# Performance work log

Hardware: AMD Instinct MI355X
Metric: run time of the kernel (lower is better)

## Reference

```python
import jax, jax.numpy as jnp
import numpy as np

VAT = 57      # vat_tokens
ACT = 56      # action_num (KV slice start for cross-attn)
H = 16        # num_heads
NG = 3        # n_groups for num_non_act == 768


def setup_inputs() -> dict:
    key = jax.random.key(0)
    ks = jax.random.split(key, 6)
    B, N, C = 64, 825, 1024
    s = 0.02
    return {
        "x": jax.random.normal(ks[0], (B, N, C), dtype=jnp.float32),
        "W_qkv_non": jax.random.normal(ks[1], (C, 3 * C), dtype=jnp.float32) * s,
        "W_q_act": jax.random.normal(ks[2], (C, C), dtype=jnp.float32) * s,
        "W_kv_act": jax.random.normal(ks[3], (C, 2 * C), dtype=jnp.float32) * s,
        "W_proj_non": jax.random.normal(ks[4], (C, C), dtype=jnp.float32) * s,
        "b_proj_non": jnp.zeros((C,), dtype=jnp.float32),
        "W_proj_act": jax.random.normal(ks[5], (C, C), dtype=jnp.float32) * s,
        "b_proj_act": jnp.zeros((C,), dtype=jnp.float32),
    }


def reference(x, W_qkv_non, W_q_act, W_kv_act, W_proj_non, b_proj_non,
              W_proj_act, b_proj_act):
    B, N, C = x.shape
    d = C // H
    scale = d ** -0.5
    nna = N - VAT              # num non-act tokens (768)
    gs = nna // NG             # group size (256)

    # --- grouped windowed self-attention over non-act tokens ---
    non = x[:, VAT:].reshape(B, NG, gs, C)
    qkv = (non @ W_qkv_non).reshape(B, NG, gs, 3, H, d)
    q, k, v = jnp.moveaxis(qkv, 3, 0)           # each [B, NG, gs, H, d]
    q = q.transpose(0, 1, 3, 2, 4)              # [B, NG, H, gs, d]
    k = k.transpose(0, 1, 3, 2, 4)
    v = v.transpose(0, 1, 3, 2, 4)
    attn = jax.nn.softmax(jnp.einsum('bghqd,bghkd->bghqk', q, k) * scale, axis=-1)
    x_non = jnp.einsum('bghqk,bghkd->bghqd', attn, v)
    x_non = x_non.transpose(0, 1, 3, 2, 4).reshape(B, nna, C)

    # --- cross-attention: act queries attend to KV subset [ACT:] of all tokens ---
    q_act = (x[:, :VAT] @ W_q_act).reshape(B, VAT, H, d).transpose(0, 2, 1, 3)
    kv = (x @ W_kv_act).reshape(B, N, 2, H, d)
    k_act = kv[:, ACT:, 0].transpose(0, 2, 1, 3)   # [B, H, N-ACT, d]
    v_act = kv[:, ACT:, 1].transpose(0, 2, 1, 3)
    attn_a = jax.nn.softmax(jnp.einsum('bhqd,bhkd->bhqk', q_act, k_act) * scale, axis=-1)
    x_act = jnp.einsum('bhqk,bhkd->bhqd', attn_a, v_act)
    x_act = x_act.transpose(0, 2, 1, 3).reshape(B, VAT, C)

    # --- output projections + concat [act, non] ---
    x_non = x_non @ W_proj_non + b_proj_non
    x_act = x_act @ W_proj_act + b_proj_act
    return jnp.concatenate([x_act, x_non], axis=1)
```

## Files before the change

kernel.cpp:

```cpp
#include <hip/hip_runtime.h>
#include <stdint.h>


typedef __attribute__((ext_vector_type(8))) unsigned short u16x8;
typedef __attribute__((ext_vector_type(8))) _Float16 f16x8;
typedef __attribute__((ext_vector_type(4))) float f32x4;

__device__ __forceinline__ unsigned short f2h(float f) {
  _Float16 h = (_Float16)f;
  return __builtin_bit_cast(unsigned short, h);
}

__device__ __forceinline__ float exp2r(float x) {
  return __builtin_amdgcn_exp2f(x);
}

__device__ __forceinline__ void mfma16(f32x4& d, u16x8 a, u16x8 b) {
  d = __builtin_amdgcn_mfma_f32_16x16x32_f16(
      __builtin_bit_cast(f16x8, a), __builtin_bit_cast(f16x8, b), d, 0, 0, 0);
}

__device__ __forceinline__ void async16(void* lds_p, const void* g) {
  __builtin_amdgcn_global_load_lds(
      (const __attribute__((address_space(1))) unsigned int*)g,
      (__attribute__((address_space(3))) unsigned int*)lds_p, 16, 0, 0);
}

__device__ __forceinline__ int swz(int row, int bcol) {
  return (row << 7) + (bcol ^ ((row & 7) << 4));
}

__device__ __forceinline__ int xcd_swz(int bid, int nwg) {
  int q8 = nwg >> 3, r8 = nwg & 7;
  int xcd = bid & 7, idx = bid >> 3;
  return (xcd < r8 ? xcd * (q8 + 1) : r8 * (q8 + 1) + (xcd - r8) * q8) + idx;
}

static constexpr size_t OFF_XB   = 0;
static constexpr size_t OFF_QKV  = 108134400;
static constexpr size_t OFF_KV   = 410124288;
static constexpr size_t OFF_QACT = 611713024;
static constexpr size_t OFF_ANON = 619184128;
static constexpr size_t OFF_AACT = 719847424;
static constexpr size_t OFF_WQKV = 727318528;
static constexpr size_t OFF_WKV  = 733609984;
static constexpr size_t OFF_WQ   = 737804288;
static constexpr size_t OFF_WPN  = 739901440;
static constexpr size_t OFF_WPA  = 741998592;

__global__ __launch_bounds__(256) void k_cast(const float* __restrict__ in,
                                              unsigned short* __restrict__ outp,
                                              int n8) {
  int stride = gridDim.x * 256;
  for (int i = blockIdx.x * 256 + threadIdx.x; i < n8; i += stride) {
    float4 v0 = ((const float4*)in)[i * 2];
    float4 v1 = ((const float4*)in)[i * 2 + 1];
    uint4 w;
    w.x = (unsigned)f2h(v0.x) | ((unsigned)f2h(v0.y) << 16);
    w.y = (unsigned)f2h(v0.z) | ((unsigned)f2h(v0.w) << 16);
    w.z = (unsigned)f2h(v1.x) | ((unsigned)f2h(v1.y) << 16);
    w.w = (unsigned)f2h(v1.z) | ((unsigned)f2h(v1.w) << 16);
    ((uint4*)outp)[i] = w;
  }
}

__global__ __launch_bounds__(256) void k_tc5(
    const float* __restrict__ Wqkv, const float* __restrict__ Wkv,
    const float* __restrict__ Wq,   const float* __restrict__ Wpn,
    const float* __restrict__ Wpa,
    unsigned short* __restrict__ Tqkv, unsigned short* __restrict__ Tkv,
    unsigned short* __restrict__ Tq,   unsigned short* __restrict__ Tpn,
    unsigned short* __restrict__ Tpa) {
  __shared__ float ts[32][33];
  int bx = blockIdx.x;
  const float* W; unsigned short* Wt; int Nc, nb;
  if (bx < 96)       { W = Wqkv; Wt = Tqkv; Nc = 3072; nb = bx; }
  else if (bx < 160) { W = Wkv;  Wt = Tkv;  Nc = 2048; nb = bx - 96; }
  else if (bx < 192) { W = Wq;   Wt = Tq;   Nc = 1024; nb = bx - 160; }
  else if (bx < 224) { W = Wpn;  Wt = Tpn;  Nc = 1024; nb = bx - 192; }
  else               { W = Wpa;  Wt = Tpa;  Nc = 1024; nb = bx - 224; }
  int n0 = nb * 32, k0 = blockIdx.y * 32;
  int tx = threadIdx.x & 31, ty = threadIdx.x >> 5;
#pragma unroll
  for (int i = 0; i < 4; i++) {
    int k = ty + i * 8;
    ts[k][tx] = W[(size_t)(k0 + k) * Nc + n0 + tx];
  }
  __syncthreads();
#pragma unroll
  for (int i = 0; i < 4; i++) {
    int n = ty + i * 8;
    Wt[(size_t)(n0 + n) * 1024 + k0 + tx] = f2h(ts[tx][n]);
  }
}

template <int EPI>
__device__ __forceinline__ void gemm256_body(
    const unsigned short* __restrict__ A, const unsigned short* __restrict__ Bt,
    const float* __restrict__ bias, void* __restrict__ outp,
    int M, int NTN, int arpb, int aoff, int ldo, int orpb, int ooff,
    int wg, char* lds) {
  int tid = threadIdx.x, lane = tid & 63, wid = tid >> 6;
  int fr = lane & 15, fg = lane >> 4;

  int mt = wg / NTN, nt = wg - mt * NTN;
  int r0 = mt << 8, n0 = nt << 8;
  if (r0 > M - 256) r0 = M - 256;

  const unsigned short* pA[2][2];
  const unsigned short* pB[2][2];
#pragma unroll
  for (int j = 0; j < 2; j++) {
    int rc = (wid * 2 + j) * 8 + (lane >> 3);
    int cc = (lane & 7) ^ (rc & 7);
#pragma unroll
    for (int a = 0; a < 2; a++) {
      int row = (rc >> 6) * 128 + a * 64 + (rc & 63);
      int r = r0 + row;
      if (r >= M) r = M - 1;
      size_t gr;
      if (arpb > 0) { int bb = r / arpb; gr = (size_t)bb * 825 + aoff + (r - bb * arpb); }
      else gr = (size_t)r;
      pA[a][j] = A + gr * 1024 + cc * 8;
    }
#pragma unroll
    for (int b = 0; b < 2; b++) {
      int n = ((rc >> 5) & 3) * 64 + b * 32 + (rc & 31);
      pB[b][j] = Bt + (size_t)(n0 + n) * 1024 + cc * 8;
    }
  }

  int wr = wid >> 2, wc = wid & 3;
  int ch0 = fg ^ (fr & 7);
  int aoff0 = (wr * 64 + fr) * 128 + ch0 * 16;
  int boff0 = (wc * 32 + fr) * 128 + ch0 * 16;

  u16x8 afr[8], bf0[4], bf1[4];
  f32x4 acc[8][4] = {};

#define BAR  asm volatile("s_barrier" ::: "memory")
#define VM6  asm volatile("s_waitcnt vmcnt(6)" ::: "memory")
#define VM0  asm volatile("s_waitcnt vmcnt(0)" ::: "memory")

  auto LDA = [&](int d, int a) {
    char* base = lds + d * 65536 + a * 16384;
#pragma unroll
    for (int mm = 0; mm < 4; mm++)
#pragma unroll
      for (int ks = 0; ks < 2; ks++)
        afr[mm * 2 + ks] = *(const u16x8*)(base + mm * 2048 + (aoff0 ^ (ks * 64)));
  };
  auto LDB = [&](int d, int b, u16x8* bf) {
    char* base = lds + d * 65536 + 32768 + b * 16384;
#pragma unroll
    for (int nn = 0; nn < 2; nn++)
#pragma unroll
      for (int ks = 0; ks < 2; ks++)
        bf[nn * 2 + ks] = *(const u16x8*)(base + nn * 2048 + (boff0 ^ (ks * 64)));
  };
  auto STAGE_A = [&](int d, int a, int t) {
#pragma unroll
    for (int j = 0; j < 2; j++)
      async16(lds + d * 65536 + a * 16384 + ((wid * 2 + j) << 10), pA[a][j] + t * 64);
  };
  auto STAGE_B = [&](int d, int b, int t) {
#pragma unroll
    for (int j = 0; j < 2; j++)
      async16(lds + d * 65536 + 32768 + b * 16384 + ((wid * 2 + j) << 10), pB[b][j] + t * 64);
  };
  auto CLUSTER = [&](int a, int b, u16x8* bf) {
    __builtin_amdgcn_s_setprio(1);
#pragma unroll
    for (int mm = 0; mm < 4; mm++)
#pragma unroll
      for (int nn = 0; nn < 2; nn++)
#pragma unroll
        for (int ks = 0; ks < 2; ks++)
          mfma16(acc[a * 4 + mm][b * 2 + nn], afr[mm * 2 + ks], bf[nn * 2 + ks]);
    __builtin_amdgcn_s_setprio(0);
  };

  STAGE_A(0, 0, 0); STAGE_B(0, 0, 0); STAGE_B(0, 1, 0); STAGE_A(0, 1, 0);
  STAGE_A(1, 0, 1); STAGE_B(1, 0, 1); STAGE_B(1, 1, 1);
  VM6; BAR;

#pragma unroll 1
  for (int i = 0; i < 8; i++) {
    bool nl = (i < 7);
    int t1 = 2 * i + 1, t2 = 2 * i + 2, t3 = 2 * i + 3;
    LDA(0, 0); LDB(0, 0, bf0);
    STAGE_A(1, 1, t1);
    CLUSTER(0, 0, bf0); BAR;
    LDB(0, 1, bf1);
    if (nl) STAGE_A(0, 0, t2);
    CLUSTER(0, 1, bf1);
    LDA(0, 1);
    if (nl) STAGE_B(0, 0, t2);
    CLUSTER(1, 0, bf0); BAR;
    if (nl) STAGE_B(0, 1, t2);
    CLUSTER(1, 1, bf1);
    if (nl) { VM6; } else { VM0; }
    BAR;
    LDA(1, 0); LDB(1, 0, bf0);
    if (nl) STAGE_A(0, 1, t2);
    CLUSTER(0, 0, bf0); BAR;
    LDB(1, 1, bf1);
    if (nl) STAGE_A(1, 0, t3);
    CLUSTER(0, 1, bf1);
    LDA(1, 1);
    if (nl) STAGE_B(1, 0, t3);
    CLUSTER(1, 0, bf0); BAR;
    if (nl) STAGE_B(1, 1, t3);
    CLUSTER(1, 1, bf1);
    if (nl) { VM6; } else { VM0; }
    BAR;
  }
#undef BAR
#undef VM6
#undef VM0

  int coln[4];
#pragma unroll
  for (int n = 0; n < 4; n++)
    coln[n] = n0 + wc * 64 + (n >> 1) * 32 + (n & 1) * 16 + fr;
  if (EPI == 0) {
    unsigned short* o = (unsigned short*)outp;
#pragma unroll
    for (int m = 0; m < 8; m++)
#pragma unroll
      for (int reg = 0; reg < 4; reg++) {
        int r = r0 + wr * 128 + (m >> 2) * 64 + (m & 3) * 16 + (lane >> 4) * 4 + reg;
        if (r < M) {
          size_t base = (size_t)r * ldo;
#pragma unroll
          for (int n = 0; n < 4; n++) o[base + coln[n]] = f2h(acc[m][n][reg]);
        }
      }
  } else {
    float* o = (float*)outp;
#pragma unroll
    for (int m = 0; m < 8; m++)
#pragma unroll
      for (int reg = 0; reg < 4; reg++) {
        int r = r0 + wr * 128 + (m >> 2) * 64 + (m & 3) * 16 + (lane >> 4) * 4 + reg;
        if (r < M) {
          int bb = r / orpb;
          size_t orow = (size_t)bb * 825 + ooff + (r - bb * orpb);
          size_t base = orow * 1024;
#pragma unroll
          for (int n = 0; n < 4; n++)
            o[base + coln[n]] = acc[m][n][reg] + bias[coln[n]];
        }
      }
  }
}

__global__ __launch_bounds__(512, 2) void k_gemm_in(
    const unsigned short* __restrict__ xb,
    const unsigned short* __restrict__ WtQKV,
    const unsigned short* __restrict__ WtKV,
    const unsigned short* __restrict__ WtQ,
    unsigned short* __restrict__ qkv, unsigned short* __restrict__ kvb,
    unsigned short* __restrict__ qact) {
  extern __shared__ char lds[];
  int bid = blockIdx.x;
  if (bid < 2304) {
    gemm256_body<0>(xb, WtQKV, nullptr, qkv, 49152, 12, 768, 57, 3072, 0, 0,
                    xcd_swz(bid, 2304), lds);
  } else if (bid < 3848) {
    gemm256_body<0>(xb, WtKV, nullptr, kvb, 49216, 8, 769, 56, 2048, 0, 0,
                    xcd_swz(bid - 2304, 1544), lds);
  } else {
    gemm256_body<0>(xb, WtQ, nullptr, qact, 3648, 4, 57, 0, 1024, 0, 0,
                    xcd_swz(bid - 3848, 60), lds);
  }
}

template <int EPI>
__global__ __launch_bounds__(512, 2) void k_gemm256(
    const unsigned short* __restrict__ A, const unsigned short* __restrict__ Bt,
    const float* __restrict__ bias, void* __restrict__ outp,
    int M, int NTN, int arpb, int aoff, int ldo, int orpb, int ooff) {
  extern __shared__ char lds[];
  gemm256_body<EPI>(A, Bt, bias, outp, M, NTN, arpb, aoff, ldo, orpb, ooff,
                    xcd_swz(blockIdx.x, gridDim.x), lds);
}

template <int EPI>
__global__ __launch_bounds__(256, 2) void k_gemm(
    const unsigned short* __restrict__ A, const unsigned short* __restrict__ Bt,
    const float* __restrict__ bias, void* __restrict__ outp,
    int M, int Nn, int arpb, int aoff, int ldo, int orpb, int ooff) {
  __shared__ __align__(16) unsigned short As[128 * 32];
  __shared__ __align__(16) unsigned short Bs[128 * 32];
  int tid = threadIdx.x, lane = tid & 63, wid = tid >> 6;
  int NT = Nn >> 7;
  int mt = blockIdx.x / NT, nt = blockIdx.x - mt * NT;
  int r0 = mt << 7, n0 = nt << 7;

  const unsigned short* aptr[2];
  const unsigned short* bptr[2];
#pragma unroll
  for (int i = 0; i < 2; i++) {
    int c = tid + (i << 8);
    int r = r0 + (c >> 2);
    if (r >= M) r = M - 1;
    size_t gr;
    if (arpb > 0) { int bb = r / arpb; gr = (size_t)bb * 825 + aoff + (r - bb * arpb); }
    else gr = (size_t)r;
    aptr[i] = A + gr * 1024 + (c & 3) * 8;
    bptr[i] = Bt + (size_t)(n0 + (c >> 2)) * 1024 + (c & 3) * 8;
  }
  char* AsB = (char*)As;
  char* BsB = (char*)Bs;
  int wr = wid >> 1, wc = wid & 1;
  int fr = lane & 15, fcol = (lane >> 4) * 16;
  f32x4 acc[4][4] = {};

  for (int kk = 0; kk < 1024; kk += 32) {
    async16(AsB + (wid << 10), aptr[0] + kk);
    async16(AsB + 4096 + (wid << 10), aptr[1] + kk);
    async16(BsB + (wid << 10), bptr[0] + kk);
    async16(BsB + 4096 + (wid << 10), bptr[1] + kk);
    __syncthreads();
    u16x8 af[4], bfv[4];
#pragma unroll
    for (int m = 0; m < 4; m++)
      af[m] = *(const u16x8*)(AsB + (wr * 64 + m * 16 + fr) * 64 + fcol);
#pragma unroll
    for (int n = 0; n < 4; n++)
      bfv[n] = *(const u16x8*)(BsB + (wc * 64 + n * 16 + fr) * 64 + fcol);
#pragma unroll
    for (int m = 0; m < 4; m++)
#pragma unroll
      for (int n = 0; n < 4; n++) mfma16(acc[m][n], af[m], bfv[n]);
    __syncthreads();
  }

  int cb = wc * 64 + fr;
  int rb = wr * 64 + (lane >> 4) * 4;
  if (EPI == 0) {
    unsigned short* o = (unsigned short*)outp;
#pragma unroll
    for (int m = 0; m < 4; m++)
#pragma unroll
      for (int reg = 0; reg < 4; reg++) {
        int r = r0 + rb + m * 16 + reg;
        if (r < M) {
          size_t base = (size_t)r * ldo + n0 + cb;
#pragma unroll
          for (int n = 0; n < 4; n++) o[base + n * 16] = f2h(acc[m][n][reg]);
        }
      }
  } else {
    float* o = (float*)outp;
#pragma unroll
    for (int m = 0; m < 4; m++)
#pragma unroll
      for (int reg = 0; reg < 4; reg++) {
        int r = r0 + rb + m * 16 + reg;
        if (r < M) {
          int bb = r / orpb;
          size_t orow = (size_t)bb * 825 + ooff + (r - bb * orpb);
          size_t base = orow * 1024 + n0 + cb;
#pragma unroll
          for (int n = 0; n < 4; n++)
            o[base + n * 16] = acc[m][n][reg] + bias[n0 + cb + n * 16];
        }
      }
  }
}

__global__ __launch_bounds__(256, 2) void k_attn_non(
    const unsigned short* __restrict__ qkv, unsigned short* __restrict__ aout) {
  int bid = blockIdx.x;
  int h = bid & 15, t = bid >> 4;
  int g = t % 3, b = t / 3;
  int tid = threadIdx.x, lane = tid & 63, wid = tid >> 6;
  int fr = lane & 15, fg = lane >> 4;
  size_t rowbase = (size_t)(b * 768 + g * 256);
  const unsigned short* Qb = qkv + rowbase * 3072 + h * 64;
  const unsigned short* Kb = Qb + 1024;
  const unsigned short* Vb = Qb + 2048;

  __shared__ __align__(16) unsigned short Vts[64 * 64];
  __shared__ __align__(16) unsigned short Ps[4][64 * 64];
  char* VtB = (char*)Vts;
  char* Pw = (char*)Ps[wid];

  int qr = wid * 64;
  u16x8 qf[4][2];
#pragma unroll
  for (int mq = 0; mq < 4; mq++)
#pragma unroll
    for (int ks = 0; ks < 2; ks++)
      qf[mq][ks] = *(const u16x8*)(Qb + (size_t)(qr + mq * 16 + fr) * 3072 + ks * 32 + fg * 8);

  f32x4 o[4][4] = {};
  float mrun[4], lrun[4];
#pragma unroll
  for (int mq = 0; mq < 4; mq++) { mrun[mq] = -1e30f; lrun[mq] = 0.f; }
  const float c1 = 0.125f * 1.44269504089f;

  int vpr = tid >> 3, vcc = tid & 7;
  u16x8 v0 = *(const u16x8*)(Vb + (size_t)(2 * vpr) * 3072 + vcc * 8);
  u16x8 v1 = *(const u16x8*)(Vb + (size_t)(2 * vpr + 1) * 3072 + vcc * 8);
  u16x8 kf[2][4];
#pragma unroll
  for (int kt = 0; kt < 4; kt++)
#pragma unroll
    for (int ks = 0; ks < 2; ks++)
      kf[ks][kt] = *(const u16x8*)(Kb + (size_t)(kt * 16 + fr) * 3072 + ks * 32 + fg * 8);

  for (int c = 0; c < 4; c++) {
    __syncthreads();
#pragma unroll
    for (int j = 0; j < 8; j++) {
      unsigned pk = (unsigned)v0[j] | ((unsigned)v1[j] << 16);
      *(unsigned*)(VtB + swz(vcc * 8 + j, 4 * vpr)) = pk;
    }
    if (c < 3) {
      v0 = *(const u16x8*)(Vb + (size_t)((c + 1) * 64 + 2 * vpr) * 3072 + vcc * 8);
      v1 = *(const u16x8*)(Vb + (size_t)((c + 1) * 64 + 2 * vpr + 1) * 3072 + vcc * 8);
    }

    f32x4 s[4][4] = {};
#pragma unroll
    for (int ks = 0; ks < 2; ks++)
#pragma unroll
      for (int kt = 0; kt < 4; kt++)
#pragma unroll
        for (int mq = 0; mq < 4; mq++) mfma16(s[kt][mq], kf[ks][kt], qf[mq][ks]);
    if (c < 3) {
#pragma unroll
      for (int kt = 0; kt < 4; kt++)
#pragma unroll
        for (int ks = 0; ks < 2; ks++)
          kf[ks][kt] = *(const u16x8*)(Kb + (size_t)((c + 1) * 64 + kt * 16 + fr) * 3072 + ks * 32 + fg * 8);
    }
#pragma unroll
    for (int kt = 0; kt < 4; kt++)
#pragma unroll
      for (int mq = 0; mq < 4; mq++) s[kt][mq] *= c1;

#pragma unroll
    for (int mq = 0; mq < 4; mq++) {
      float v = -1e30f;
#pragma unroll
      for (int kt = 0; kt < 4; kt++)
#pragma unroll
        for (int reg = 0; reg < 4; reg++) v = fmaxf(v, s[kt][mq][reg]);
      v = fmaxf(v, __shfl_xor(v, 16));
      v = fmaxf(v, __shfl_xor(v, 32));
      float mn = fmaxf(mrun[mq], v);
      float alpha = exp2r(mrun[mq] - mn);
      mrun[mq] = mn;
      int q = mq * 16 + fr;
      float rs = 0.f;
#pragma unroll
      for (int kt = 0; kt < 4; kt++) {
        f32x4 p;
#pragma unroll
        for (int reg = 0; reg < 4; reg++) p[reg] = exp2r(s[kt][mq][reg] - mn);
        rs += p[0] + p[1] + p[2] + p[3];
        uint2 w;
        w.x = (unsigned)f2h(p[0]) | ((unsigned)f2h(p[1]) << 16);
        w.y = (unsigned)f2h(p[2]) | ((unsigned)f2h(p[3]) << 16);
        *(uint2*)(Pw + swz(q, kt * 32 + fg * 8)) = w;
      }
      rs += __shfl_xor(rs, 16);
      rs += __shfl_xor(rs, 32);
      lrun[mq] = lrun[mq] * alpha + rs;
#pragma unroll
      for (int dt = 0; dt < 4; dt++) o[dt][mq] *= alpha;
    }
    __syncthreads();
#pragma unroll
    for (int ks = 0; ks < 2; ks++) {
      u16x8 vf[4], pf[4];
#pragma unroll
      for (int dt = 0; dt < 4; dt++)
        vf[dt] = *(const u16x8*)(VtB + swz(dt * 16 + fr, ks * 64 + fg * 16));
#pragma unroll
      for (int mq = 0; mq < 4; mq++)
        pf[mq] = *(const u16x8*)(Pw + swz(mq * 16 + fr, ks * 64 + fg * 16));
#pragma unroll
      for (int dt = 0; dt < 4; dt++)
#pragma unroll
        for (int mq = 0; mq < 4; mq++) mfma16(o[dt][mq], vf[dt], pf[mq]);
    }
  }

#pragma unroll
  for (int mq = 0; mq < 4; mq++) {
    float rl = 1.0f / lrun[mq];
    size_t row = rowbase + qr + mq * 16 + fr;
#pragma unroll
    for (int dt = 0; dt < 4; dt++) {
      uint2 w;
      w.x = (unsigned)f2h(o[dt][mq][0] * rl) | ((unsigned)f2h(o[dt][mq][1] * rl) << 16);
      w.y = (unsigned)f2h(o[dt][mq][2] * rl) | ((unsigned)f2h(o[dt][mq][3] * rl) << 16);
      *(uint2*)(aout + row * 1024 + h * 64 + dt * 16 + fg * 4) = w;
    }
  }
}

__global__ __launch_bounds__(256, 2) void k_attn_act(
    const unsigned short* __restrict__ qa, const unsigned short* __restrict__ kv,
    unsigned short* __restrict__ aout) {
  int bid = blockIdx.x;
  int h = bid & 15, b = bid >> 4;
  int tid = threadIdx.x, lane = tid & 63, wid = tid >> 6;
  int fr = lane & 15, fg = lane >> 4;
  const unsigned short* Qb = qa + (size_t)b * 57 * 1024 + h * 64;
  const unsigned short* Kb = kv + (size_t)b * 769 * 2048 + h * 64;
  const unsigned short* Vb = Kb + 1024;

  __shared__ __align__(16) unsigned short Vts[4][64 * 64];
  __shared__ __align__(16) unsigned short Ps[4][64 * 64];
  __shared__ float Ml[4][64], Ll[4][64];
  char* Vw = (char*)Vts[wid];
  char* Pw = (char*)Ps[wid];

  u16x8 qf[4][2];
#pragma unroll
  for (int mq = 0; mq < 4; mq++) {
    int q = mq * 16 + fr;
    if (q > 56) q = 56;
#pragma unroll
    for (int ks = 0; ks < 2; ks++)
      qf[mq][ks] = *(const u16x8*)(Qb + (size_t)q * 1024 + ks * 32 + fg * 8);
  }
  f32x4 o[4][4] = {};
  float mrun[4], lrun[4];
#pragma unroll
  for (int mq = 0; mq < 4; mq++) { mrun[mq] = -1e30f; lrun[mq] = 0.f; }
  const float c1 = 0.125f * 1.44269504089f;

  u16x8 kf[2][4];
  {
    int kc0 = wid * 64;
#pragma unroll
    for (int kt = 0; kt < 4; kt++) {
      int krow = kc0 + kt * 16 + fr;
      if (krow > 768) krow = 768;
#pragma unroll
      for (int ks = 0; ks < 2; ks++)
        kf[ks][kt] = *(const u16x8*)(Kb + (size_t)krow * 2048 + ks * 32 + fg * 8);
    }
  }

  for (int c = wid; c < 13; c += 4) {
    int kc0 = c * 64;
#pragma unroll
    for (int i = 0; i < 4; i++) {
      int idx = lane + i * 64;
      int pr = idx >> 3, cv = idx & 7;
      int kr0 = kc0 + 2 * pr, kr1 = kc0 + 2 * pr + 1;
      if (kr0 > 768) kr0 = 768;
      if (kr1 > 768) kr1 = 768;
      u16x8 v0 = *(const u16x8*)(Vb + (size_t)kr0 * 2048 + cv * 8);
      u16x8 v1 = *(const u16x8*)(Vb + (size_t)kr1 * 2048 + cv * 8);
#pragma unroll
      for (int j = 0; j < 8; j++) {
        unsigned pk = (unsigned)v0[j] | ((unsigned)v1[j] << 16);
        *(unsigned*)(Vw + swz(cv * 8 + j, 4 * pr)) = pk;
      }
    }

    f32x4 s[4][4] = {};
#pragma unroll
    for (int ks = 0; ks < 2; ks++)
#pragma unroll
      for (int kt = 0; kt < 4; kt++)
#pragma unroll
        for (int mq = 0; mq < 4; mq++) mfma16(s[kt][mq], kf[ks][kt], qf[mq][ks]);
    if (c + 4 < 13) {
      int kn = (c + 4) * 64;
#pragma unroll
      for (int kt = 0; kt < 4; kt++) {
        int krow = kn + kt * 16 + fr;
        if (krow > 768) krow = 768;
#pragma unroll
        for (int ks = 0; ks < 2; ks++)
          kf[ks][kt] = *(const u16x8*)(Kb + (size_t)krow * 2048 + ks * 32 + fg * 8);
      }
    }
#pragma unroll
    for (int kt = 0; kt < 4; kt++)
#pragma unroll
      for (int mq = 0; mq < 4; mq++) s[kt][mq] *= c1;
    if (kc0 + 64 > 769) {
#pragma unroll
      for (int kt = 0; kt < 4; kt++)
#pragma unroll
        for (int reg = 0; reg < 4; reg++)
          if (kc0 + kt * 16 + fg * 4 + reg >= 769)
#pragma unroll
            for (int mq = 0; mq < 4; mq++) s[kt][mq][reg] = -1e30f;
    }

#pragma unroll
    for (int mq = 0; mq < 4; mq++) {
      float v = -1e30f;
#pragma unroll
      for (int kt = 0; kt < 4; kt++)
#pragma unroll
        for (int reg = 0; reg < 4; reg++) v = fmaxf(v, s[kt][mq][reg]);
      v = fmaxf(v, __shfl_xor(v, 16));
      v = fmaxf(v, __shfl_xor(v, 32));
      float mn = fmaxf(mrun[mq], v);
      float alpha = exp2r(mrun[mq] - mn);
      mrun[mq] = mn;
      int q = mq * 16 + fr;
      float rs = 0.f;
#pragma unroll
      for (int kt = 0; kt < 4; kt++) {
        f32x4 p;
#pragma unroll
        for (int reg = 0; reg < 4; reg++) p[reg] = exp2r(s[kt][mq][reg] - mn);
        rs += p[0] + p[1] + p[2] + p[3];
        uint2 w;
        w.x = (unsigned)f2h(p[0]) | ((unsigned)f2h(p[1]) << 16);
        w.y = (unsigned)f2h(p[2]) | ((unsigned)f2h(p[3]) << 16);
        *(uint2*)(Pw + swz(q, kt * 32 + fg * 8)) = w;
      }
      rs += __shfl_xor(rs, 16);
      rs += __shfl_xor(rs, 32);
      lrun[mq] = lrun[mq] * alpha + rs;
#pragma unroll
      for (int dt = 0; dt < 4; dt++) o[dt][mq] *= alpha;
    }
#pragma unroll
    for (int ks = 0; ks < 2; ks++) {
      u16x8 vf[4], pf[4];
#pragma unroll
      for (int dt = 0; dt < 4; dt++)
        vf[dt] = *(const u16x8*)(Vw + swz(dt * 16 + fr, ks * 64 + fg * 16));
#pragma unroll
      for (int mq = 0; mq < 4; mq++)
        pf[mq] = *(const u16x8*)(Pw + swz(mq * 16 + fr, ks * 64 + fg * 16));
#pragma unroll
      for (int dt = 0; dt < 4; dt++)
#pragma unroll
        for (int mq = 0; mq < 4; mq++) mfma16(o[dt][mq], vf[dt], pf[mq]);
    }
  }

  __syncthreads();
  if (fg == 0) {
#pragma unroll
    for (int mq = 0; mq < 4; mq++) {
      Ml[wid][mq * 16 + fr] = mrun[mq];
      Ll[wid][mq * 16 + fr] = lrun[mq];
    }
  }
  __syncthreads();
  float* Oac = (float*)&Vts[0][0];
  for (int i = tid; i < 4096; i += 256) Oac[i] = 0.f;
  __syncthreads();
  for (int w = 0; w < 4; w++) {
    if (wid == w) {
#pragma unroll
      for (int mq = 0; mq < 4; mq++) {
        int q = mq * 16 + fr;
        float Mq = fmaxf(fmaxf(Ml[0][q], Ml[1][q]), fmaxf(Ml[2][q], Ml[3][q]));
        float f = exp2r(mrun[mq] - Mq);
#pragma unroll
        for (int dt = 0; dt < 4; dt++) {
          int d = dt * 16 + fg * 4;
#pragma unroll
          for (int reg = 0; reg < 4; reg++)
            Oac[(d + reg) * 64 + q] += o[dt][mq][reg] * f;
        }
      }
    }
    __syncthreads();
  }
  for (int i = tid; i < 4096; i += 256) {
    int d = i >> 6, q = i & 63;
    if (q < 57) {
      float Mq = fmaxf(fmaxf(Ml[0][q], Ml[1][q]), fmaxf(Ml[2][q], Ml[3][q]));
      float Lq = Ll[0][q] * exp2r(Ml[0][q] - Mq) + Ll[1][q] * exp2r(Ml[1][q] - Mq) +
                 Ll[2][q] * exp2r(Ml[2][q] - Mq) + Ll[3][q] * exp2r(Ml[3][q] - Mq);
      aout[(size_t)(b * 57 + q) * 1024 + h * 64 + d] = f2h(Oac[i] / Lq);
    }
  }
}

extern "C" void kernel_launch(void* const* d_in, const int* in_sizes, int n_in,
                              void* d_out, int out_size, void* d_ws, size_t ws_size,
                              hipStream_t stream) {
  const float* x    = (const float*)d_in[0];
  const float* Wqkv = (const float*)d_in[1];
  const float* Wq   = (const float*)d_in[2];
  const float* Wkv  = (const float*)d_in[3];
  const float* Wpn  = (const float*)d_in[4];
  const float* bpn  = (const float*)d_in[5];
  const float* Wpa  = (const float*)d_in[6];
  const float* bpa  = (const float*)d_in[7];
  float* out = (float*)d_out;
  char* ws = (char*)d_ws;

  unsigned short* xb   = (unsigned short*)(ws + OFF_XB);
  unsigned short* qkv  = (unsigned short*)(ws + OFF_QKV);
  unsigned short* kvb  = (unsigned short*)(ws + OFF_KV);
  unsigned short* qact = (unsigned short*)(ws + OFF_QACT);
  unsigned short* anon = (unsigned short*)(ws + OFF_ANON);
  unsigned short* aact = (unsigned short*)(ws + OFF_AACT);
  unsigned short* WtQKV = (unsigned short*)(ws + OFF_WQKV);
  unsigned short* WtKV  = (unsigned short*)(ws + OFF_WKV);
  unsigned short* WtQ   = (unsigned short*)(ws + OFF_WQ);
  unsigned short* WtPN  = (unsigned short*)(ws + OFF_WPN);
  unsigned short* WtPA  = (unsigned short*)(ws + OFF_WPA);

  hipFuncSetAttribute((const void*)k_gemm_in,
                      hipFuncAttributeMaxDynamicSharedMemorySize, 131072);
  hipFuncSetAttribute((const void*)k_gemm256<1>,
                      hipFuncAttributeMaxDynamicSharedMemorySize, 131072);

  k_cast<<<2048, 256, 0, stream>>>(x, xb, 6758400);
  k_tc5<<<dim3(256, 32), 256, 0, stream>>>(Wqkv, Wkv, Wq, Wpn, Wpa,
                                           WtQKV, WtKV, WtQ, WtPN, WtPA);

  k_gemm_in<<<3908, 512, 131072, stream>>>(xb, WtQKV, WtKV, WtQ,
                                           qkv, kvb, qact);

  k_attn_non<<<64 * 3 * 16, 256, 0, stream>>>(qkv, anon);
  k_attn_act<<<64 * 16, 256, 0, stream>>>(qact, kvb, aact);

  k_gemm256<1><<<192 * 4, 512, 131072, stream>>>(anon, WtPN, bpn, out,
                                                 49152, 4, 0, 0, 1024, 768, 57);
  k_gemm<1><<<29 * 8, 256, 0, stream>>>(aact, WtPA, bpa, out,
                                        3648, 1024, 0, 0, 1024, 57, 0);
}
```

Before: 980.6 us.

## Double-buffer V tile, lazy softmax rescale, and remap V transpose threads

The non-act attention kernel now keeps two LDS buffers for the transposed V tile, so the next tile is written while the current one is consumed, and the second barrier per iteration is dropped. Both attention kernels skip the online-softmax rescale of the output and sum when the new max exceeds the running max by at most 8 (log2 units), which relies on fp16 P values staying in range. The lane-to-(row,column) mapping for the V transpose is changed, which alters LDS write and global load access patterns. This trades extra LDS and a wave-uniform branch for fewer barriers and fewer exp/multiply operations.

```diff
diff --git a/kernel.cpp b/kernel.cpp
--- a/kernel.cpp
+++ b/kernel.cpp
@@ -383,9 +383,8 @@
   const unsigned short* Kb = Qb + 1024;
   const unsigned short* Vb = Qb + 2048;
 
-  __shared__ __align__(16) unsigned short Vts[64 * 64];
+  __shared__ __align__(16) unsigned short Vts[2][64 * 64];
   __shared__ __align__(16) unsigned short Ps[4][64 * 64];
-  char* VtB = (char*)Vts;
   char* Pw = (char*)Ps[wid];
 
   int qr = wid * 64;
@@ -402,9 +401,12 @@
   for (int mq = 0; mq < 4; mq++) { mrun[mq] = -1e30f; lrun[mq] = 0.f; }
   const float c1 = 0.125f * 1.44269504089f;
 
-  int vpr = tid >> 3, vcc = tid & 7;
-  u16x8 v0 = *(const u16x8*)(Vb + (size_t)(2 * vpr) * 3072 + vcc * 8);
-  u16x8 v1 = *(const u16x8*)(Vb + (size_t)(2 * vpr + 1) * 3072 + vcc * 8);
+  int vpr = lane & 31;
+  int vcc = wid * 2 + (lane >> 5);
+  const unsigned short* Vp = Vb + (size_t)(2 * vpr) * 3072 + vcc * 8;
+
+  u16x8 v0 = *(const u16x8*)(Vp);
+  u16x8 v1 = *(const u16x8*)(Vp + 3072);
   u16x8 kf[2][4];
 #pragma unroll
   for (int kt = 0; kt < 4; kt++)
@@ -412,16 +414,30 @@
     for (int ks = 0; ks < 2; ks++)
       kf[ks][kt] = *(const u16x8*)(Kb + (size_t)(kt * 16 + fr) * 3072 + ks * 32 + fg * 8);
 
+  {
+    char* VtN = (char*)Vts[0];
+#pragma unroll
+    for (int j = 0; j < 8; j++) {
+      unsigned pk = (unsigned)v0[j] | ((unsigned)v1[j] << 16);
+      *(unsigned*)(VtN + swz(vcc * 8 + j, 4 * vpr)) = pk;
+    }
+    v0 = *(const u16x8*)(Vp + (size_t)64 * 3072);
+    v1 = *(const u16x8*)(Vp + (size_t)65 * 3072);
+  }
+
   for (int c = 0; c < 4; c++) {
     __syncthreads();
-#pragma unroll
-    for (int j = 0; j < 8; j++) {
-      unsigned pk = (unsigned)v0[j] | ((unsigned)v1[j] << 16);
-      *(unsigned*)(VtB + swz(vcc * 8 + j, 4 * vpr)) = pk;
-    }
     if (c < 3) {
-      v0 = *(const u16x8*)(Vb + (size_t)((c + 1) * 64 + 2 * vpr) * 3072 + vcc * 8);
-      v1 = *(const u16x8*)(Vb + (size_t)((c + 1) * 64 + 2 * vpr + 1) * 3072 + vcc * 8);
+      char* VtN = (char*)Vts[(c + 1) & 1];
+#pragma unroll
+      for (int j = 0; j < 8; j++) {
+        unsigned pk = (unsigned)v0[j] | ((unsigned)v1[j] << 16);
+        *(unsigned*)(VtN + swz(vcc * 8 + j, 4 * vpr)) = pk;
+      }
+      if (c < 2) {
+        v0 = *(const u16x8*)(Vp + (size_t)(c + 2) * 64 * 3072);
+        v1 = *(const u16x8*)(Vp + (size_t)((c + 2) * 64 + 1) * 3072);
+      }
     }
 
     f32x4 s[4][4] = {};
@@ -452,9 +468,15 @@
         for (int reg = 0; reg < 4; reg++) v = fmaxf(v, s[kt][mq][reg]);
       v = fmaxf(v, __shfl_xor(v, 16));
       v = fmaxf(v, __shfl_xor(v, 32));
-      float mn = fmaxf(mrun[mq], v);
-      float alpha = exp2r(mrun[mq] - mn);
-      mrun[mq] = mn;
+      if (!__all(v <= mrun[mq] + 8.f)) {
+        float mn = fmaxf(mrun[mq], v);
+        float alpha = exp2r(mrun[mq] - mn);
+        mrun[mq] = mn;
+        lrun[mq] *= alpha;
+#pragma unroll
+        for (int dt = 0; dt < 4; dt++) o[dt][mq] *= alpha;
+      }
+      float mn = mrun[mq];
       int q = mq * 16 + fr;
       float rs = 0.f;
 #pragma unroll
@@ -470,11 +492,9 @@
       }
       rs += __shfl_xor(rs, 16);
       rs += __shfl_xor(rs, 32);
-      lrun[mq] = lrun[mq] * alpha + rs;
-#pragma unroll
-      for (int dt = 0; dt < 4; dt++) o[dt][mq] *= alpha;
-    }
-    __syncthreads();
+      lrun[mq] += rs;
+    }
+    char* VtB = (char*)Vts[c & 1];
 #pragma unroll
     for (int ks = 0; ks < 2; ks++) {
       u16x8 vf[4], pf[4];
@@ -550,13 +570,13 @@
     }
   }
 
+  int vpr = lane & 31;
   for (int c = wid; c < 13; c += 4) {
     int kc0 = c * 64;
 #pragma unroll
     for (int i = 0; i < 4; i++) {
-      int idx = lane + i * 64;
-      int pr = idx >> 3, cv = idx & 7;
-      int kr0 = kc0 + 2 * pr, kr1 = kc0 + 2 * pr + 1;
+      int cv = i * 2 + (lane >> 5);
+      int kr0 = kc0 + 2 * vpr, kr1 = kc0 + 2 * vpr + 1;
       if (kr0 > 768) kr0 = 768;
       if (kr1 > 768) kr1 = 768;
       u16x8 v0 = *(const u16x8*)(Vb + (size_t)kr0 * 2048 + cv * 8);
@@ -564,7 +584,7 @@
 #pragma unroll
       for (int j = 0; j < 8; j++) {
         unsigned pk = (unsigned)v0[j] | ((unsigned)v1[j] << 16);
-        *(unsigned*)(Vw + swz(cv * 8 + j, 4 * pr)) = pk;
+        *(unsigned*)(Vw + swz(cv * 8 + j, 4 * vpr)) = pk;
       }
     }
 
@@ -609,9 +629,15 @@
         for (int reg = 0; reg < 4; reg++) v = fmaxf(v, s[kt][mq][reg]);
       v = fmaxf(v, __shfl_xor(v, 16));
       v = fmaxf(v, __shfl_xor(v, 32));
-      float mn = fmaxf(mrun[mq], v);
-      float alpha = exp2r(mrun[mq] - mn);
-      mrun[mq] = mn;
+      if (!__all(v <= mrun[mq] + 8.f)) {
+        float mn = fmaxf(mrun[mq], v);
+        float alpha = exp2r(mrun[mq] - mn);
+        mrun[mq] = mn;
+        lrun[mq] *= alpha;
+#pragma unroll
+        for (int dt = 0; dt < 4; dt++) o[dt][mq] *= alpha;
+      }
+      float mn = mrun[mq];
       int q = mq * 16 + fr;
       float rs = 0.f;
 #pragma unroll
@@ -627,9 +653,7 @@
       }
       rs += __shfl_xor(rs, 16);
       rs += __shfl_xor(rs, 32);
-      lrun[mq] = lrun[mq] * alpha + rs;
-#pragma unroll
-      for (int dt = 0; dt < 4; dt++) o[dt][mq] *= alpha;
+      lrun[mq] += rs;
     }
 #pragma unroll
     for (int ks = 0; ks < 2; ks++) {
```

After: 941.8 us. -3.9%, faster.
